# Kernel optimization log

Measured on AMD Instinct MI355X. Metric: run time of the kernel, lower is better.

Reference implementation:

```python
import jax, jax.numpy as jnp
import numpy as np

N_HEAD, D_MODEL, D_K, D_V = 4, 512, 128, 128
B, LQ, LK = 1024, 32, 64
EPS = 1e-5


def setup_inputs() -> dict:
    key = jax.random.key(0)
    ks = jax.random.split(key, 10)
    s = 0.02
    q = jax.random.normal(ks[0], (B, LQ, D_MODEL), jnp.float32)
    k = jax.random.normal(ks[1], (B, LK, D_MODEL), jnp.float32)
    v = jax.random.normal(ks[2], (B, LK, D_MODEL), jnp.float32)
    mask = jax.random.bernoulli(ks[3], 0.15, (B, LQ, LK))  # True = null neighbor
    Wq = jax.random.normal(ks[4], (N_HEAD * D_K, D_MODEL), jnp.float32) * s
    Wk = jax.random.normal(ks[5], (N_HEAD * D_K, D_MODEL), jnp.float32) * s
    Wv = jax.random.normal(ks[6], (N_HEAD * D_K, D_MODEL), jnp.float32) * s
    Wmap = jax.random.normal(ks[7], (1, 2 * D_K), jnp.float32) * s
    fcW = jax.random.normal(ks[8], (D_MODEL, N_HEAD * D_V), jnp.float32) * s
    fcb = jnp.zeros((D_MODEL,), jnp.float32)
    gamma = jnp.ones((D_MODEL,), jnp.float32)
    beta = jnp.zeros((D_MODEL,), jnp.float32)
    return dict(q=q, k=k, v=v, mask=mask, Wq=Wq, Wk=Wk, Wv=Wv, Wmap=Wmap,
                fcW=fcW, fcb=fcb, gamma=gamma, beta=beta)


def reference(q, k, v, mask, Wq, Wk, Wv, Wmap, fcW, fcb, gamma, beta):
    # Projections -> [B, L, H, d]
    qp = (q @ Wq.T).reshape(B, LQ, N_HEAD, D_K)
    kp = (k @ Wk.T).reshape(B, LK, N_HEAD, D_K)
    vp = (v @ Wv.T).reshape(B, LK, N_HEAD, D_V)
    # weight_map(concat(q,k)) == q . w_left + k . w_right  (exact same math,
    # avoids materializing the expanded [H*B, LQ, LK, 2*D_K] concat tensor)
    wm_q, wm_k = Wmap[0, :D_K], Wmap[0, D_K:]
    sq = jnp.einsum('bqhd,d->hbq', qp, wm_q)  # [H, B, LQ]
    sk = jnp.einsum('bkhd,d->hbk', kp, wm_k)  # [H, B, LK]
    attn = sq[:, :, :, None] + sk[:, :, None, :]  # [H, B, LQ, LK]
    attn = jnp.where(mask[None], jnp.float32(-1e10), attn)
    attn = jax.nn.softmax(attn, axis=-1)
    # dropout is identity (eval / p=0)
    out = jnp.einsum('hbqk,bkhd->bqhd', attn, vp).reshape(B, LQ, N_HEAD * D_V)
    out = jax.nn.leaky_relu(out @ fcW.T + fcb, negative_slope=0.2)
    out = out + q  # residual
    mu = out.mean(-1, keepdims=True)
    var = out.var(-1, keepdims=True)
    out = gamma * (out - mu) / jnp.sqrt(var + EPS) + beta
    return out, attn.reshape(N_HEAD * B, LQ, LK)
```

## Files before the change

kernel.cpp:

```cpp
#include <hip/hip_runtime.h>
#include <hip/hip_bf16.h>

#define NHEAD 4
#define DMODEL 512
#define DK 128
#define BB 1024
#define LQ 32
#define LK 64
#define LN_EPS 1e-5f

typedef __attribute__((ext_vector_type(8))) __bf16 bf16x8;
typedef __attribute__((ext_vector_type(8))) short short8;
typedef __attribute__((ext_vector_type(4))) float floatx4;
typedef __attribute__((ext_vector_type(4))) unsigned uintx4;

__device__ __forceinline__ float b2f(unsigned short u) {
  unsigned v = ((unsigned)u) << 16;
  return __builtin_bit_cast(float, v);
}
__device__ __forceinline__ unsigned short f2b(float f) {
  unsigned u = __builtin_bit_cast(unsigned, f);
  u += 0x7fffu + ((u >> 16) & 1u);
  return (unsigned short)(u >> 16);
}
__device__ __forceinline__ float ldS(const void* p, size_t i, int f32) {
  return f32 ? ((const float*)p)[i] : b2f(((const unsigned short*)p)[i]);
}
__device__ __forceinline__ void load8f(const void* base, size_t i8, int f32, float o[8]) {
  if (f32) {
    const float* p = (const float*)base + i8;
    float4 a = *(const float4*)p, b = *(const float4*)(p + 4);
    o[0] = a.x; o[1] = a.y; o[2] = a.z; o[3] = a.w;
    o[4] = b.x; o[5] = b.y; o[6] = b.z; o[7] = b.w;
  } else {
    short8 v = *(const short8*)((const unsigned short*)base + i8);
#pragma unroll
    for (int j = 0; j < 8; ++j) o[j] = b2f(((const unsigned short*)&v)[j]);
  }
}

__global__ void detect_kernel(const unsigned* __restrict__ gbits,
                              const unsigned* __restrict__ mbits,
                              unsigned* __restrict__ flags) {
  if (threadIdx.x == 0) flags[0] = (gbits[0] == 0x3F800000u) ? 1u : 0u;
  if (threadIdx.x == 1) {
    unsigned any = 0;
    for (int i = 0; i < 64; ++i) {
      unsigned w = mbits[i];
      if (w != 0u && w != 1u && w != 0xFFFFFFFFu) any = 1;
    }
    flags[1] = any;
  }
}
__device__ __forceinline__ int mread(const void* m, size_t i, int m8) {
  return m8 ? (int)((const unsigned char*)m)[i] : (((const int*)m)[i] != 0);
}

__global__ __launch_bounds__(256) void convw_kernel(
    const void* __restrict__ Wv, const void* __restrict__ fcW,
    unsigned short* __restrict__ Wv_c, unsigned short* __restrict__ fcW_c,
    const unsigned* __restrict__ flags) {
  int f32 = flags[0];
  int idx = blockIdx.x * 256 + threadIdx.x;
  int sel = idx >> 15;
  size_t i8 = (size_t)(idx & 32767) * 8;
  float x[8];
  load8f(sel ? fcW : Wv, i8, f32, x);
  unsigned short o[8];
#pragma unroll
  for (int j = 0; j < 8; ++j) o[j] = f2b(x[j]);
  *(short8*)((sel ? fcW_c : Wv_c) + i8) = *(const short8*)o;
}

__global__ __launch_bounds__(256) void prep_weff(
    const void* __restrict__ Wq, const void* __restrict__ Wk,
    const void* __restrict__ Wmap,
    float* __restrict__ wq_eff, float* __restrict__ wk_eff,
    const unsigned* __restrict__ flags) {
  int f32 = flags[0];
  int idx = blockIdx.x * 256 + threadIdx.x;
  int sel = idx >> 11;
  int i = idx & 2047;
  int h = i >> 9, m = i & 511;
  const void* W = sel ? Wk : Wq;
  float acc = 0.f;
  for (int d = 0; d < DK; ++d)
    acc += ldS(W, (size_t)(h * DK + d) * DMODEL + m, f32) * ldS(Wmap, sel * DK + d, f32);
  (sel ? wk_eff : wq_eff)[i] = acc;
}

__global__ __launch_bounds__(512, 4) void fused_kernel(
    const void* __restrict__ v, const void* __restrict__ qin,
    const void* __restrict__ kin,
    const unsigned short* __restrict__ Wv_c,
    const unsigned short* __restrict__ fcW_c,
    const float* __restrict__ wq_eff, const float* __restrict__ wk_eff,
    const void* __restrict__ mask,
    const void* __restrict__ fcb, const void* __restrict__ gamma,
    const void* __restrict__ beta, void* __restrict__ d_out,
    const unsigned* __restrict__ flags) {
  int f32 = flags[0], m8 = flags[1];
  int b = blockIdx.x;
  __shared__ __align__(16) short U[64 * 520];
  __shared__ float sqs[4][32], sks[4][64];
  __shared__ float psum[8][32], psum2[8][32];
  __shared__ float rmu[32], rinv[32];
  short (*vps)[520] = (short(*)[520])U;
  short (*probs)[72] = (short(*)[72])U;
  short (*att)[520] = (short(*)[520])U;
  int tid = threadIdx.x;
  int wv = tid >> 6, lane = tid & 63, l16 = lane & 15, quad = lane >> 4;

  {
#pragma unroll 4
    for (int rr = 0; rr < 12; ++rr) {
      int r = wv * 12 + rr;
      int isq = r < 32;
      int lr = isq ? r : r - 32;
      size_t base = isq ? ((size_t)b * 32 + lr) : ((size_t)b * 64 + lr);
      float x[8];
      load8f(isq ? qin : kin, base * DMODEL + lane * 8, f32, x);
      const float* we = (isq ? wq_eff : wk_eff) + lane * 8;
      float acc[4];
#pragma unroll
      for (int h = 0; h < 4; ++h) {
        const float4* wp = (const float4*)(we + h * 512);
        float4 wa = wp[0], wb = wp[1];
        acc[h] = x[0] * wa.x + x[1] * wa.y + x[2] * wa.z + x[3] * wa.w +
                 x[4] * wb.x + x[5] * wb.y + x[6] * wb.z + x[7] * wb.w;
      }
#pragma unroll
      for (int h = 0; h < 4; ++h)
#pragma unroll
        for (int off = 32; off; off >>= 1) acc[h] += __shfl_xor(acc[h], off, 64);
      if (lane == 0) {
#pragma unroll
        for (int h = 0; h < 4; ++h)
          (isq ? &sqs[h][lr] : &sks[h][lr])[0] = acc[h];
      }
    }
  }

  for (int i = tid; i < 4096; i += 512) {
    int e = i * 8, row = e >> 9, col = e & 511;
    float x[8];
    load8f(v, (size_t)b * (64 * 512) + e, f32, x);
    unsigned short o[8];
#pragma unroll
    for (int j = 0; j < 8; ++j) o[j] = f2b(x[j]);
    *(short8*)&vps[row][col] = *(const short8*)o;
  }
  __syncthreads();

  floatx4 acc1[4][4] = {};
  for (int k0 = 0; k0 < 512; k0 += 32) {
    bf16x8 af[4], wf[4];
#pragma unroll
    for (int mf = 0; mf < 4; ++mf)
      af[mf] = __builtin_bit_cast(bf16x8, *(const short8*)&vps[mf * 16 + l16][k0 + quad * 8]);
#pragma unroll
    for (int nf = 0; nf < 4; ++nf)
      wf[nf] = __builtin_bit_cast(bf16x8,
          *(const short8*)(Wv_c + (size_t)(wv * 64 + nf * 16 + l16) * 512 + k0 + quad * 8));
#pragma unroll
    for (int mf = 0; mf < 4; ++mf)
#pragma unroll
      for (int nf = 0; nf < 4; ++nf)
        acc1[mf][nf] = __builtin_amdgcn_mfma_f32_16x16x32_bf16(af[mf], wf[nf], acc1[mf][nf], 0, 0, 0);
  }
  unsigned pk1[4][4][2];
#pragma unroll
  for (int mf = 0; mf < 4; ++mf)
#pragma unroll
    for (int nf = 0; nf < 4; ++nf) {
      pk1[mf][nf][0] = (unsigned)f2b(acc1[mf][nf][0]) | ((unsigned)f2b(acc1[mf][nf][1]) << 16);
      pk1[mf][nf][1] = (unsigned)f2b(acc1[mf][nf][2]) | ((unsigned)f2b(acc1[mf][nf][3]) << 16);
    }
  __syncthreads();

  int h = wv >> 1;
  {
    int qb = (wv & 1) * 16;
    char* abase = (char*)d_out + ((size_t)BB * LQ * DMODEL << (f32 ? 2 : 1));
    float skl = sks[h][lane];
    for (int i = 0; i < 16; ++i) {
      int qrow = qb + i;
      float s = sqs[h][qrow] + skl;
      if (mread(mask, ((size_t)b * 32 + qrow) * 64 + lane, m8)) s = -1e10f;
      float mx = s;
#pragma unroll
      for (int off = 32; off; off >>= 1) mx = fmaxf(mx, __shfl_xor(mx, off, 64));
      float p = __expf(s - mx);
      float sm = p;
#pragma unroll
      for (int off = 32; off; off >>= 1) sm += __shfl_xor(sm, off, 64);
      float pn = p / sm;
      size_t oi = ((size_t)(h * 1024 + b) * 32 + qrow) * 64 + lane;
      if (f32) ((float*)abase)[oi] = pn; else ((unsigned short*)abase)[oi] = f2b(pn);
      float pn2 = __shfl_xor(pn, 1, 64);
      if (!(lane & 1))
        *(unsigned*)&probs[h * 32 + qrow][lane] =
            (unsigned)f2b(pn) | ((unsigned)f2b(pn2) << 16);
    }
  }
  __syncthreads();

  floatx4 accp[2][4] = {};
  {
    int lo = l16 + ((quad & 1) << 5);
    int hi = lo + 16;
    int hiHalf = quad >> 1;
#pragma unroll
    for (int ks = 0; ks < 2; ++ks) {
      bf16x8 pa[2];
#pragma unroll
      for (int m2 = 0; m2 < 2; ++m2)
        pa[m2] = __builtin_bit_cast(bf16x8,
            *(const short8*)&probs[h * 32 + m2 * 16 + l16][ks * 32 + quad * 8]);
#pragma unroll
      for (int nf = 0; nf < 4; ++nf) {
        unsigned la0 = __shfl(pk1[2 * ks][nf][0], lo, 64);
        unsigned la1 = __shfl(pk1[2 * ks][nf][1], lo, 64);
        unsigned ha0 = __shfl(pk1[2 * ks][nf][0], hi, 64);
        unsigned ha1 = __shfl(pk1[2 * ks][nf][1], hi, 64);
        unsigned lb0 = __shfl(pk1[2 * ks + 1][nf][0], lo, 64);
        unsigned lb1 = __shfl(pk1[2 * ks + 1][nf][1], lo, 64);
        unsigned hb0 = __shfl(pk1[2 * ks + 1][nf][0], hi, 64);
        unsigned hb1 = __shfl(pk1[2 * ks + 1][nf][1], hi, 64);
        uintx4 bw;
        bw.x = hiHalf ? lb0 : la0;
        bw.y = hiHalf ? lb1 : la1;
        bw.z = hiHalf ? hb0 : ha0;
        bw.w = hiHalf ? hb1 : ha1;
        bf16x8 bfr = __builtin_bit_cast(bf16x8, bw);
#pragma unroll
        for (int m2 = 0; m2 < 2; ++m2)
          accp[m2][nf] = __builtin_amdgcn_mfma_f32_16x16x32_bf16(pa[m2], bfr, accp[m2][nf], 0, 0, 0);
      }
    }
  }
  __syncthreads();

#pragma unroll
  for (int m2 = 0; m2 < 2; ++m2)
#pragma unroll
    for (int nf = 0; nf < 4; ++nf)
#pragma unroll
      for (int r = 0; r < 4; ++r)
        att[m2 * 16 + quad * 4 + r][wv * 64 + nf * 16 + l16] = f2b(accp[m2][nf][r]);
  __syncthreads();

  floatx4 acc2[2][4] = {};
  for (int k0 = 0; k0 < 512; k0 += 32) {
    bf16x8 af2[2], wf2[4];
#pragma unroll
    for (int mf = 0; mf < 2; ++mf)
      af2[mf] = __builtin_bit_cast(bf16x8, *(const short8*)&att[mf * 16 + l16][k0 + quad * 8]);
#pragma unroll
    for (int nf = 0; nf < 4; ++nf)
      wf2[nf] = __builtin_bit_cast(bf16x8,
          *(const short8*)(fcW_c + (size_t)(wv * 64 + nf * 16 + l16) * 512 + k0 + quad * 8));
#pragma unroll
    for (int mf = 0; mf < 2; ++mf)
#pragma unroll
      for (int nf = 0; nf < 4; ++nf)
        acc2[mf][nf] = __builtin_amdgcn_mfma_f32_16x16x32_bf16(af2[mf], wf2[nf], acc2[mf][nf], 0, 0, 0);
  }

  float fcbv[4], gmv[4], btv[4];
#pragma unroll
  for (int nf = 0; nf < 4; ++nf) {
    int col = wv * 64 + nf * 16 + l16;
    fcbv[nf] = ldS(fcb, col, f32);
    gmv[nf] = ldS(gamma, col, f32);
    btv[nf] = ldS(beta, col, f32);
  }
#pragma unroll
  for (int mf = 0; mf < 2; ++mf)
#pragma unroll
    for (int r = 0; r < 4; ++r) {
      int rloc = mf * 16 + quad * 4 + r;
      float s = 0.f, s2 = 0.f;
#pragma unroll
      for (int nf = 0; nf < 4; ++nf) {
        int col = wv * 64 + nf * 16 + l16;
        float x = acc2[mf][nf][r] + fcbv[nf];
        x = x > 0.f ? x : 0.2f * x;
        x += ldS(qin, (size_t)(b * 32 + rloc) * 512 + col, f32);
        acc2[mf][nf][r] = x;
        s += x;
        s2 += x * x;
      }
#pragma unroll
      for (int off = 1; off < 16; off <<= 1) {
        s += __shfl_xor(s, off, 64);
        s2 += __shfl_xor(s2, off, 64);
      }
      if (l16 == 0) { psum[wv][rloc] = s; psum2[wv][rloc] = s2; }
    }
  __syncthreads();
  if (tid < 32) {
    float s = 0.f, s2 = 0.f;
#pragma unroll
    for (int w = 0; w < 8; ++w) { s += psum[w][tid]; s2 += psum2[w][tid]; }
    float mu = s * (1.f / 512.f);
    float var = s2 * (1.f / 512.f) - mu * mu;
    rmu[tid] = mu;
    rinv[tid] = rsqrtf(var + LN_EPS);
  }
  __syncthreads();
#pragma unroll
  for (int mf = 0; mf < 2; ++mf)
#pragma unroll
    for (int r = 0; r < 4; ++r) {
      int rloc = mf * 16 + quad * 4 + r;
      float mu = rmu[rloc], inv = rinv[rloc];
#pragma unroll
      for (int nf = 0; nf < 4; ++nf) {
        int col = wv * 64 + nf * 16 + l16;
        float y = gmv[nf] * (acc2[mf][nf][r] - mu) * inv + btv[nf];
        size_t oi = (size_t)(b * 32 + rloc) * 512 + col;
        if (f32) ((float*)d_out)[oi] = y; else ((unsigned short*)d_out)[oi] = f2b(y);
      }
    }
}

extern "C" void kernel_launch(void* const* d_in, const int* in_sizes, int n_in,
                              void* d_out, int out_size, void* d_ws, size_t ws_size,
                              hipStream_t stream) {
  const void* q = d_in[0];
  const void* k = d_in[1];
  const void* v = d_in[2];
  const void* mask = d_in[3];
  const void* Wq = d_in[4];
  const void* Wk = d_in[5];
  const void* Wv = d_in[6];
  const void* Wmap = d_in[7];
  const void* fcW = d_in[8];
  const void* fcb = d_in[9];
  const void* gamma = d_in[10];
  const void* beta = d_in[11];

  char* ws = (char*)d_ws;
  unsigned short* Wv_c = (unsigned short*)ws;
  unsigned short* fcW_c = (unsigned short*)(ws + 524288);
  float* wq_eff = (float*)(ws + 1048576);
  float* wk_eff = (float*)(ws + 1056768);
  unsigned* flags = (unsigned*)(ws + 2637824);
  const size_t REQUIRED = 2637888ull;
  if (ws_size < REQUIRED) return;

  detect_kernel<<<1, 64, 0, stream>>>((const unsigned*)gamma, (const unsigned*)mask, flags);
  convw_kernel<<<256, 256, 0, stream>>>(Wv, fcW, Wv_c, fcW_c, flags);
  prep_weff<<<16, 256, 0, stream>>>(Wq, Wk, Wmap, wq_eff, wk_eff, flags);
  fused_kernel<<<BB, 512, 0, stream>>>(v, q, k, Wv_c, fcW_c, wq_eff, wk_eff, mask,
                                       fcb, gamma, beta, d_out, flags);
}
```

Measured before the change: 547.8 us.

## Merge prep kernels, inline dtype detection, and bitpack mask into shared memory

Folds the detect, weight-convert and effective-weight kernels into one prep launch, and moves dtype/mask-format detection into the fused kernel, which removes two launches and the flags buffer. The fused kernel now loads each mask row once, ballots it into a 64-bit bitmask in shared memory, and reads the bits in the softmax loop instead of doing per-element global mask loads. It also lowers the launch_bounds minimum-blocks hint from 4 to 2, giving the compiler more register room at a possible cost in occupancy.

Result: slower. 578.0 us (+5.5%).

```diff
diff --git a/kernel.cpp b/kernel.cpp
--- a/kernel.cpp
+++ b/kernel.cpp
@@ -38,58 +38,43 @@
     for (int j = 0; j < 8; ++j) o[j] = b2f(((const unsigned short*)&v)[j]);
   }
 }
-
-__global__ void detect_kernel(const unsigned* __restrict__ gbits,
-                              const unsigned* __restrict__ mbits,
-                              unsigned* __restrict__ flags) {
-  if (threadIdx.x == 0) flags[0] = (gbits[0] == 0x3F800000u) ? 1u : 0u;
-  if (threadIdx.x == 1) {
-    unsigned any = 0;
-    for (int i = 0; i < 64; ++i) {
-      unsigned w = mbits[i];
-      if (w != 0u && w != 1u && w != 0xFFFFFFFFu) any = 1;
-    }
-    flags[1] = any;
-  }
-}
 __device__ __forceinline__ int mread(const void* m, size_t i, int m8) {
   return m8 ? (int)((const unsigned char*)m)[i] : (((const int*)m)[i] != 0);
 }
 
-__global__ __launch_bounds__(256) void convw_kernel(
+__global__ __launch_bounds__(256) void prep_kernel(
     const void* __restrict__ Wv, const void* __restrict__ fcW,
-    unsigned short* __restrict__ Wv_c, unsigned short* __restrict__ fcW_c,
-    const unsigned* __restrict__ flags) {
-  int f32 = flags[0];
-  int idx = blockIdx.x * 256 + threadIdx.x;
-  int sel = idx >> 15;
-  size_t i8 = (size_t)(idx & 32767) * 8;
-  float x[8];
-  load8f(sel ? fcW : Wv, i8, f32, x);
-  unsigned short o[8];
-#pragma unroll
-  for (int j = 0; j < 8; ++j) o[j] = f2b(x[j]);
-  *(short8*)((sel ? fcW_c : Wv_c) + i8) = *(const short8*)o;
-}
-
-__global__ __launch_bounds__(256) void prep_weff(
     const void* __restrict__ Wq, const void* __restrict__ Wk,
     const void* __restrict__ Wmap,
+    unsigned short* __restrict__ Wv_c, unsigned short* __restrict__ fcW_c,
     float* __restrict__ wq_eff, float* __restrict__ wk_eff,
-    const unsigned* __restrict__ flags) {
-  int f32 = flags[0];
-  int idx = blockIdx.x * 256 + threadIdx.x;
-  int sel = idx >> 11;
-  int i = idx & 2047;
-  int h = i >> 9, m = i & 511;
-  const void* W = sel ? Wk : Wq;
-  float acc = 0.f;
-  for (int d = 0; d < DK; ++d)
-    acc += ldS(W, (size_t)(h * DK + d) * DMODEL + m, f32) * ldS(Wmap, sel * DK + d, f32);
-  (sel ? wk_eff : wq_eff)[i] = acc;
-}
-
-__global__ __launch_bounds__(512, 4) void fused_kernel(
+    const unsigned* __restrict__ gbits) {
+  int f32 = (gbits[0] == 0x3F800000u) ? 1 : 0;
+  int bid = blockIdx.x;
+  if (bid < 256) {
+    int idx = bid * 256 + threadIdx.x;
+    int sel = idx >> 15;
+    size_t i8 = (size_t)(idx & 32767) * 8;
+    float x[8];
+    load8f(sel ? fcW : Wv, i8, f32, x);
+    unsigned short o[8];
+#pragma unroll
+    for (int j = 0; j < 8; ++j) o[j] = f2b(x[j]);
+    *(short8*)((sel ? fcW_c : Wv_c) + i8) = *(const short8*)o;
+  } else {
+    int idx = (bid - 256) * 256 + threadIdx.x;
+    int sel = idx >> 11;
+    int i = idx & 2047;
+    int h = i >> 9, m = i & 511;
+    const void* W = sel ? Wk : Wq;
+    float acc = 0.f;
+    for (int d = 0; d < DK; ++d)
+      acc += ldS(W, (size_t)(h * DK + d) * DMODEL + m, f32) * ldS(Wmap, sel * DK + d, f32);
+    (sel ? wk_eff : wq_eff)[i] = acc;
+  }
+}
+
+__global__ __launch_bounds__(512, 2) void fused_kernel(
     const void* __restrict__ v, const void* __restrict__ qin,
     const void* __restrict__ kin,
     const unsigned short* __restrict__ Wv_c,
@@ -97,19 +82,31 @@
     const float* __restrict__ wq_eff, const float* __restrict__ wk_eff,
     const void* __restrict__ mask,
     const void* __restrict__ fcb, const void* __restrict__ gamma,
-    const void* __restrict__ beta, void* __restrict__ d_out,
-    const unsigned* __restrict__ flags) {
-  int f32 = flags[0], m8 = flags[1];
+    const void* __restrict__ beta, void* __restrict__ d_out) {
   int b = blockIdx.x;
   __shared__ __align__(16) short U[64 * 520];
   __shared__ float sqs[4][32], sks[4][64];
   __shared__ float psum[8][32], psum2[8][32];
   __shared__ float rmu[32], rinv[32];
+  __shared__ unsigned long long umask[32];
   short (*vps)[520] = (short(*)[520])U;
   short (*probs)[72] = (short(*)[72])U;
   short (*att)[520] = (short(*)[520])U;
   int tid = threadIdx.x;
   int wv = tid >> 6, lane = tid & 63, l16 = lane & 15, quad = lane >> 4;
+
+  int f32 = (((const unsigned*)gamma)[0] == 0x3F800000u) ? 1 : 0;
+  unsigned mw = ((const unsigned*)mask)[lane];
+  unsigned long long bad = __ballot(mw != 0u && mw != 1u && mw != 0xFFFFFFFFu);
+  int m8 = (bad != 0ull) ? 1 : 0;
+
+#pragma unroll
+  for (int j = 0; j < 4; ++j) {
+    int row = wv * 4 + j;
+    int mv = mread(mask, ((size_t)b * 32 + row) * 64 + lane, m8);
+    unsigned long long bm = __ballot(mv != 0);
+    if (lane == 0) umask[row] = bm;
+  }
 
   {
 #pragma unroll 4
@@ -185,8 +182,9 @@
     float skl = sks[h][lane];
     for (int i = 0; i < 16; ++i) {
       int qrow = qb + i;
+      unsigned long long mrow = umask[qrow];
       float s = sqs[h][qrow] + skl;
-      if (mread(mask, ((size_t)b * 32 + qrow) * 64 + lane, m8)) s = -1e10f;
+      if ((mrow >> lane) & 1ull) s = -1e10f;
       float mx = s;
 #pragma unroll
       for (int off = 32; off; off >>= 1) mx = fmaxf(mx, __shfl_xor(mx, off, 64));
@@ -346,13 +344,11 @@
   unsigned short* fcW_c = (unsigned short*)(ws + 524288);
   float* wq_eff = (float*)(ws + 1048576);
   float* wk_eff = (float*)(ws + 1056768);
-  unsigned* flags = (unsigned*)(ws + 2637824);
-  const size_t REQUIRED = 2637888ull;
+  const size_t REQUIRED = 1064960ull;
   if (ws_size < REQUIRED) return;
 
-  detect_kernel<<<1, 64, 0, stream>>>((const unsigned*)gamma, (const unsigned*)mask, flags);
-  convw_kernel<<<256, 256, 0, stream>>>(Wv, fcW, Wv_c, fcW_c, flags);
-  prep_weff<<<16, 256, 0, stream>>>(Wq, Wk, Wmap, wq_eff, wk_eff, flags);
+  prep_kernel<<<272, 256, 0, stream>>>(Wv, fcW, Wq, Wk, Wmap, Wv_c, fcW_c,
+                                       wq_eff, wk_eff, (const unsigned*)gamma);
   fused_kernel<<<BB, 512, 0, stream>>>(v, q, k, Wv_c, fcW_c, wq_eff, wk_eff, mask,
-                                       fcb, gamma, beta, d_out, flags);
-}
+                                       fcb, gamma, beta, d_out);
+}
```
